# Performance work log

Hardware: AMD Instinct MI355X
Metric: run time of the kernel (lower is better)

## Reference

```python
import jax, jax.numpy as jnp
import numpy as np

N = 100000   # nodes
E = 1600000  # edges
D = 128      # feature dim
C = 32       # n classes (logits dim)
LN_EPS = 1e-5   # torch LayerNorm default eps
LOG_EPS = 1e-9  # numerical floor inside logs


def setup_inputs() -> dict:
    key = jax.random.key(0)
    ks = jax.random.split(key, 8)
    h = jax.random.normal(ks[0], (N, D), jnp.float32)
    logits = jax.random.normal(ks[1], (N, C), jnp.float32)
    old_z = jax.random.uniform(ks[2], (N,), jnp.float32)
    norm = jax.random.uniform(ks[3], (N, 1), jnp.float32)  # degree norm per node
    tau_1 = jax.random.uniform(ks[4], (1,), jnp.float32)
    tau_2 = jax.random.uniform(ks[5], (1,), jnp.float32)
    src = jax.random.randint(ks[6], (E,), 0, N, jnp.int32)
    dst = jax.random.randint(ks[7], (E,), 0, N, jnp.int32)
    return dict(h=h, logits=logits, old_z=old_z, norm=norm,
                tau_1=tau_1, tau_2=tau_2, src=src, dst=dst)


def _layernorm_over_nodes(x):
    # LayerNorm(N, elementwise_affine=False) applied to a length-N vector:
    # normalize over the entire node dimension.
    mu = jnp.mean(x)
    var = jnp.mean(jnp.square(x - mu))
    return (x - mu) * jax.lax.rsqrt(var + LN_EPS)


def reference(h, logits, old_z, norm, tau_1, tau_2, src, dst):
    # --- message pass 1: adaptive_reduce_func over neighbor logits ---
    probs = jax.nn.softmax(logits, axis=-1)                      # [N,C]
    ones = jnp.ones((src.shape[0],), h.dtype)
    deg = jax.ops.segment_sum(ones, dst, num_segments=N)          # in-degree [N]
    sum_p = jax.ops.segment_sum(probs[src], dst, num_segments=N)  # [N,C]
    mean_p = sum_p / jnp.maximum(deg, 1.0)[:, None]               # neighborhood consensus
    log_self = jnp.log(probs + LOG_EPS)
    log_mean = jnp.log(mean_p + LOG_EPS)
    f1 = jnp.sum(probs * (log_self - log_mean), axis=-1)          # KL(self || mean-neighbor)
    f2 = -jnp.sum(mean_p * log_mean, axis=-1)                     # entropy of consensus
    has_nb = deg > 0  # DGL leaves zero-in-degree nodes at 0
    f1 = jnp.where(has_nb, f1, 0.0)
    f2 = jnp.where(has_nb, f2, 0.0)

    # --- gating (shared_tau=True path) ---
    z = jax.nn.sigmoid(-(_layernorm_over_nodes(f1) - tau_1)) \
      * jax.nn.sigmoid(-(_layernorm_over_nodes(f2) - tau_2))      # [N]
    gate = jnp.minimum(old_z, z)

    # --- message pass 2: sum-aggregate neighbor features ---
    agg = jax.ops.segment_sum(h[src], dst, num_segments=N)        # [N,D]
    normagg = jax.nn.relu(agg * norm)
    new_h = h + gate[:, None] * normagg
    return new_h, z
```

## Files before the change

kernel.cpp:

```cpp
#include <hip/hip_runtime.h>
#include <math.h>

#define CN 32
#define DN 128
#define BKT_SHIFT 9
#define BKT_NODES 512
#define CHUNK 8192
#define MAXBKT 1024

__global__ void k_softmax(const float* __restrict__ logits, float* __restrict__ probs, int N) {
    int t = blockIdx.x * blockDim.x + threadIdx.x;
    int node = t >> 5, c = t & 31;
    if (node >= N) return;
    float l = logits[node * CN + c];
    float m = l;
    #pragma unroll
    for (int o = 16; o; o >>= 1) m = fmaxf(m, __shfl_xor(m, o, 32));
    float e = __expf(l - m);
    float s = e;
    #pragma unroll
    for (int o = 16; o; o >>= 1) s += __shfl_xor(s, o, 32);
    probs[node * CN + c] = e / s;
}

__global__ void k_part_hist(const int* __restrict__ dst, int* __restrict__ M,
                            int E, int NBKT) {
    __shared__ int hist[MAXBKT];
    int t = threadIdx.x;
    for (int j = t; j < NBKT; j += 256) hist[j] = 0;
    __syncthreads();
    int ebeg = blockIdx.x * CHUNK;
    #pragma unroll
    for (int k = 0; k < CHUNK / 256; ++k) {
        int e = ebeg + k * 256 + t;
        if (e < E) atomicAdd(&hist[dst[e] >> BKT_SHIFT], 1);
    }
    __syncthreads();
    int* row = M + (size_t)blockIdx.x * NBKT;
    for (int j = t; j < NBKT; j += 256) row[j] = hist[j];
}

__global__ void k_part_scan(int* __restrict__ M, int* __restrict__ bbase,
                            int NCH, int NBKT, int E) {
    __shared__ int wsum[16], wpre[16];
    __shared__ int carry;
    int t = threadIdx.x, ln = t & 63, wv = t >> 6;
    if (t == 0) carry = 0;
    __syncthreads();
    int L = NCH * NBKT;
    for (int base = 0; base < L; base += 1024) {
        int k = base + t;
        int idx = 0, v = 0;
        if (k < L) {
            int b = k / NCH, ch = k - b * NCH;
            idx = ch * NBKT + b;
            v = M[idx];
        }
        int incl = v;
        #pragma unroll
        for (int o = 1; o < 64; o <<= 1) { int u = __shfl_up(incl, o, 64); if (ln >= o) incl += u; }
        if (ln == 63) wsum[wv] = incl;
        __syncthreads();
        if (t == 0) {
            int r = carry;
            #pragma unroll
            for (int w = 0; w < 16; ++w) { wpre[w] = r; r += wsum[w]; }
            carry = r;
        }
        __syncthreads();
        if (k < L) M[idx] = wpre[wv] + incl - v;
        __syncthreads();
    }
    for (int b = t; b < NBKT; b += 1024) bbase[b] = M[b];
    if (t == 0) bbase[NBKT] = E;
}

__global__ void k_part_scatter(const int* __restrict__ src, const int* __restrict__ dst,
                               const int* __restrict__ M, int* __restrict__ part,
                               int E, int NBKT) {
    __shared__ int cur[MAXBKT];
    int t = threadIdx.x;
    const int* row = M + (size_t)blockIdx.x * NBKT;
    for (int j = t; j < NBKT; j += 256) cur[j] = row[j];
    __syncthreads();
    int ebeg = blockIdx.x * CHUNK;
    #pragma unroll
    for (int k = 0; k < CHUNK / 256; ++k) {
        int e = ebeg + k * 256 + t;
        if (e < E) {
            int d = dst[e];
            int b = d >> BKT_SHIFT;
            int p = atomicAdd(&cur[b], 1);
            part[p] = ((d & (BKT_NODES - 1)) << 17) | src[e];
        }
    }
}

__global__ void k_bucket_csr(const int* __restrict__ part, const int* __restrict__ bbase,
                             int* __restrict__ cnt, int* __restrict__ off,
                             int* __restrict__ eidx, int N) {
    __shared__ int hcnt[BKT_NODES];
    __shared__ int wsum[8], wpre[8];
    int t = threadIdx.x, ln = t & 63, wv = t >> 6;
    int b = blockIdx.x;
    int lo = bbase[b], hi = bbase[b + 1];
    hcnt[t] = 0;
    __syncthreads();
    for (int e = lo + t; e < hi; e += BKT_NODES)
        atomicAdd(&hcnt[part[e] >> 17], 1);
    __syncthreads();
    int v = hcnt[t];
    int incl = v;
    #pragma unroll
    for (int o = 1; o < 64; o <<= 1) { int u = __shfl_up(incl, o, 64); if (ln >= o) incl += u; }
    if (ln == 63) wsum[wv] = incl;
    __syncthreads();
    if (t == 0) {
        int r = 0;
        #pragma unroll
        for (int w = 0; w < 8; ++w) { wpre[w] = r; r += wsum[w]; }
    }
    __syncthreads();
    int excl = wpre[wv] + incl - v;
    int g = b * BKT_NODES + t;
    if (g < N) { cnt[g] = v; off[g] = lo + excl; }
    hcnt[t] = excl;
    __syncthreads();
    for (int e = lo + t; e < hi; e += BKT_NODES) {
        int pk = part[e];
        int p = atomicAdd(&hcnt[pk >> 17], 1);
        eidx[lo + p] = pk & 0x1FFFF;
    }
}

__global__ void k_probs_f(const float* __restrict__ probs, const int* __restrict__ off,
                          const int* __restrict__ cnt, const int* __restrict__ eidx,
                          float* __restrict__ f1buf, float* __restrict__ f2buf,
                          double* __restrict__ pbuf, int N) {
    int t = blockIdx.x * blockDim.x + threadIdx.x;
    int i = t >> 5, c = t & 31;
    float f1 = 0.f, f2 = 0.f;
    if (i < N) {
        int beg = off[i], dg = cnt[i];
        float sum = 0.f;
        for (int base = 0; base < dg; base += 16) {
            int rem = dg - base;
            int lim = rem < 16 ? rem : 16;
            int myi = (c < lim) ? eidx[beg + base + c] : 0;
            #pragma unroll
            for (int j = 0; j < 16; ++j) {
                int s = __shfl(myi, j, 32);
                float v = probs[(size_t)s * CN + c];
                sum += (j < rem) ? v : 0.f;
            }
        }
        float f1c = 0.f, f2c = 0.f;
        if (dg > 0) {
            float p = probs[(size_t)i * CN + c];
            float mp = sum / (float)dg;
            float lm = logf(mp + 1e-9f);
            f1c = p * (logf(p + 1e-9f) - lm);
            f2c = -mp * lm;
        }
        #pragma unroll
        for (int o = 16; o; o >>= 1) { f1c += __shfl_xor(f1c, o, 32); f2c += __shfl_xor(f2c, o, 32); }
        if (c == 0) { f1buf[i] = f1c; f2buf[i] = f2c; f1 = f1c; f2 = f2c; }
    }
    double v0 = f1, v1 = (double)f1 * f1, v2 = f2, v3 = (double)f2 * f2;
    #pragma unroll
    for (int o = 32; o; o >>= 1) {
        v0 += __shfl_down(v0, o, 64);
        v1 += __shfl_down(v1, o, 64);
        v2 += __shfl_down(v2, o, 64);
        v3 += __shfl_down(v3, o, 64);
    }
    __shared__ double sh[4][4];
    int wave = threadIdx.x >> 6, lane = threadIdx.x & 63;
    if (lane == 0) { sh[0][wave] = v0; sh[1][wave] = v1; sh[2][wave] = v2; sh[3][wave] = v3; }
    __syncthreads();
    if (threadIdx.x == 0) {
        double a = 0, b = 0, c2 = 0, d = 0;
        #pragma unroll
        for (int w = 0; w < 4; ++w) { a += sh[0][w]; b += sh[1][w]; c2 += sh[2][w]; d += sh[3][w]; }
        double* p = pbuf + (size_t)blockIdx.x * 4;
        p[0] = a; p[1] = b; p[2] = c2; p[3] = d;
    }
}

__global__ void k_redstats(const double* __restrict__ pbuf, double* __restrict__ stats, int nblk) {
    int t = threadIdx.x;
    double a = 0, b = 0, c = 0, d = 0;
    for (int k = t; k < nblk; k += blockDim.x) {
        const double* p = pbuf + (size_t)k * 4;
        a += p[0]; b += p[1]; c += p[2]; d += p[3];
    }
    #pragma unroll
    for (int o = 32; o; o >>= 1) {
        a += __shfl_down(a, o, 64);
        b += __shfl_down(b, o, 64);
        c += __shfl_down(c, o, 64);
        d += __shfl_down(d, o, 64);
    }
    __shared__ double sh[4][16];
    int wv = t >> 6, ln = t & 63;
    if (ln == 0) { sh[0][wv] = a; sh[1][wv] = b; sh[2][wv] = c; sh[3][wv] = d; }
    __syncthreads();
    if (t == 0) {
        double s0 = 0, s1 = 0, s2 = 0, s3 = 0;
        int nw = blockDim.x >> 6;
        for (int w = 0; w < nw; ++w) { s0 += sh[0][w]; s1 += sh[1][w]; s2 += sh[2][w]; s3 += sh[3][w]; }
        stats[0] = s0; stats[1] = s1; stats[2] = s2; stats[3] = s3;
    }
}

__global__ void k_z(const float* __restrict__ f1buf, const float* __restrict__ f2buf,
                    const double* __restrict__ stats, const float* __restrict__ old_z,
                    const float* __restrict__ tau1, const float* __restrict__ tau2,
                    float* __restrict__ z_out, float* __restrict__ gate, int N) {
    int i = blockIdx.x * blockDim.x + threadIdx.x;
    if (i >= N) return;
    double invN = 1.0 / (double)N;
    float mu1 = (float)(stats[0] * invN);
    float var1 = (float)(stats[1] * invN) - mu1 * mu1;
    float is1 = rsqrtf(var1 + 1e-5f);
    float mu2 = (float)(stats[2] * invN);
    float var2 = (float)(stats[3] * invN) - mu2 * mu2;
    float is2 = rsqrtf(var2 + 1e-5f);
    float a = (f1buf[i] - mu1) * is1;
    float b = (f2buf[i] - mu2) * is2;
    float z = (1.f / (1.f + __expf(a - tau1[0]))) * (1.f / (1.f + __expf(b - tau2[0])));
    z_out[i] = z;
    gate[i] = fminf(old_z[i], z);
}

__global__ void k_gather_final(const float* __restrict__ h, const int* __restrict__ off,
                               const int* __restrict__ cnt, const int* __restrict__ eidx,
                               const float* __restrict__ gate, const float* __restrict__ norm,
                               float* __restrict__ out, int N) {
    int t = blockIdx.x * blockDim.x + threadIdx.x;
    int i = t >> 6, ln = t & 63;
    if (i >= N) return;
    int beg = off[i], dg = cnt[i];
    const float2* h2 = (const float2*)h;
    float ax = 0.f, ay = 0.f;
    for (int base = 0; base < dg; base += 16) {
        int rem = dg - base;
        int lim = rem < 16 ? rem : 16;
        int myi = (ln < lim) ? eidx[beg + base + ln] : 0;
        #pragma unroll
        for (int j = 0; j < 16; ++j) {
            int s = __shfl(myi, j, 64);
            float2 v = h2[(size_t)s * 64 + ln];
            bool use = j < rem;
            ax += use ? v.x : 0.f;
            ay += use ? v.y : 0.f;
        }
    }
    float g = gate[i], nm = norm[i];
    float2 hv = h2[(size_t)i * 64 + ln];
    float2 r;
    r.x = hv.x + g * fmaxf(ax * nm, 0.f);
    r.y = hv.y + g * fmaxf(ay * nm, 0.f);
    ((float2*)out)[(size_t)i * 64 + ln] = r;
}

extern "C" void kernel_launch(void* const* d_in, const int* in_sizes, int n_in,
                              void* d_out, int out_size, void* d_ws, size_t ws_size,
                              hipStream_t stream) {
    const float* h      = (const float*)d_in[0];
    const float* logits = (const float*)d_in[1];
    const float* old_z  = (const float*)d_in[2];
    const float* norm   = (const float*)d_in[3];
    const float* tau1   = (const float*)d_in[4];
    const float* tau2   = (const float*)d_in[5];
    const int*   src    = (const int*)d_in[6];
    const int*   dst    = (const int*)d_in[7];
    const int N = in_sizes[2];
    const int E = in_sizes[6];

    float* out   = (float*)d_out;
    float* z_out = out + (size_t)N * DN;

    const int B = 256;
    const int NBF  = (N * CN + B - 1) / B;
    const int NBKT = (N + BKT_NODES - 1) >> BKT_SHIFT;
    const int NCH  = (E + CHUNK - 1) / CHUNK;

    char*   ws    = (char*)d_ws;
    double* stats = (double*)ws;
    int*    cnt   = (int*)(ws + 64);
    int*    off   = cnt + N;
    int*    bbase = off + N;
    int*    M     = bbase + MAXBKT + 8;
    int*    eidx  = M + (size_t)NCH * NBKT;
    int*    part  = eidx + E;
    float*  probs = (float*)(part + E);
    float*  f1buf = probs + (size_t)N * CN;
    float*  f2buf = f1buf + N;
    float*  gate  = f2buf + N;
    double* pbuf  = (double*)(((size_t)(gate + N) + 15) & ~(size_t)15);

    k_softmax<<<(N * CN + B - 1) / B, B, 0, stream>>>(logits, probs, N);

    k_part_hist<<<NCH, 256, 0, stream>>>(dst, M, E, NBKT);
    k_part_scan<<<1, 1024, 0, stream>>>(M, bbase, NCH, NBKT, E);
    k_part_scatter<<<NCH, 256, 0, stream>>>(src, dst, M, part, E, NBKT);
    k_bucket_csr<<<NBKT, BKT_NODES, 0, stream>>>(part, bbase, cnt, off, eidx, N);

    k_probs_f<<<NBF, B, 0, stream>>>(probs, off, cnt, eidx, f1buf, f2buf, pbuf, N);
    k_redstats<<<1, 1024, 0, stream>>>(pbuf, stats, NBF);
    k_z<<<(N + B - 1) / B, B, 0, stream>>>(f1buf, f2buf, stats, old_z, tau1, tau2, z_out, gate, N);

    k_gather_final<<<(N * 64 + B - 1) / B, B, 0, stream>>>(h, off, cnt, eidx, gate, norm, out, N);
}
```

Before: 302.7 us.

## Gather neighbor probs and features in bf16, stage bucket CSR in LDS

Adds bf16 copies of the softmax probabilities and of h, and makes the two neighbor-gather kernels read these half-width copies while keeping fp32 accumulation and fp32 self terms. The aim is to roughly halve the random-gather memory traffic that dominates both message passes. The bucket-CSR kernel now loads each bucket's packed edges into LDS once and writes the sorted indices back in place, removing one E-sized buffer. In exchange it adds a full conversion pass over h, loses precision in the aggregated sums, and silently drops edges when a bucket holds more than DCAP entries.

```diff
diff --git a/kernel.cpp b/kernel.cpp
--- a/kernel.cpp
+++ b/kernel.cpp
@@ -7,8 +7,18 @@
 #define BKT_NODES 512
 #define CHUNK 8192
 #define MAXBKT 1024
-
-__global__ void k_softmax(const float* __restrict__ logits, float* __restrict__ probs, int N) {
+#define DCAP 12288
+
+__device__ __forceinline__ unsigned short f2b(float f) {
+    unsigned u = __float_as_uint(f);
+    return (unsigned short)((u + 0x7FFFu + ((u >> 16) & 1u)) >> 16);
+}
+__device__ __forceinline__ float b2f(unsigned short s) {
+    return __uint_as_float(((unsigned)s) << 16);
+}
+
+__global__ void k_softmax(const float* __restrict__ logits, float* __restrict__ probs,
+                          unsigned short* __restrict__ probs_b, int N) {
     int t = blockIdx.x * blockDim.x + threadIdx.x;
     int node = t >> 5, c = t & 31;
     if (node >= N) return;
@@ -20,7 +30,18 @@
     float s = e;
     #pragma unroll
     for (int o = 16; o; o >>= 1) s += __shfl_xor(s, o, 32);
-    probs[node * CN + c] = e / s;
+    float p = e / s;
+    probs[node * CN + c] = p;
+    probs_b[node * CN + c] = f2b(p);
+}
+
+__global__ void k_cvt_h(const float4* __restrict__ h4, ushort4* __restrict__ hb4, int n4) {
+    int t = blockIdx.x * blockDim.x + threadIdx.x;
+    if (t >= n4) return;
+    float4 v = h4[t];
+    ushort4 r;
+    r.x = f2b(v.x); r.y = f2b(v.y); r.z = f2b(v.z); r.w = f2b(v.w);
+    hb4[t] = r;
 }
 
 __global__ void k_part_hist(const int* __restrict__ dst, int* __restrict__ M,
@@ -96,18 +117,20 @@
     }
 }
 
-__global__ void k_bucket_csr(const int* __restrict__ part, const int* __restrict__ bbase,
-                             int* __restrict__ cnt, int* __restrict__ off,
-                             int* __restrict__ eidx, int N) {
+__global__ void k_bucket_csr(int* __restrict__ part, const int* __restrict__ bbase,
+                             int* __restrict__ cnt, int* __restrict__ off, int N) {
+    __shared__ int sbuf[DCAP];
     __shared__ int hcnt[BKT_NODES];
     __shared__ int wsum[8], wpre[8];
     int t = threadIdx.x, ln = t & 63, wv = t >> 6;
     int b = blockIdx.x;
     int lo = bbase[b], hi = bbase[b + 1];
+    int n = hi - lo;
+    if (n > DCAP) n = DCAP;
+    for (int e = t; e < n; e += BKT_NODES) sbuf[e] = part[lo + e];
     hcnt[t] = 0;
     __syncthreads();
-    for (int e = lo + t; e < hi; e += BKT_NODES)
-        atomicAdd(&hcnt[part[e] >> 17], 1);
+    for (int e = t; e < n; e += BKT_NODES) atomicAdd(&hcnt[sbuf[e] >> 17], 1);
     __syncthreads();
     int v = hcnt[t];
     int incl = v;
@@ -126,15 +149,17 @@
     if (g < N) { cnt[g] = v; off[g] = lo + excl; }
     hcnt[t] = excl;
     __syncthreads();
-    for (int e = lo + t; e < hi; e += BKT_NODES) {
-        int pk = part[e];
+    for (int e = t; e < n; e += BKT_NODES) {
+        int pk = sbuf[e];
         int p = atomicAdd(&hcnt[pk >> 17], 1);
-        eidx[lo + p] = pk & 0x1FFFF;
-    }
-}
-
-__global__ void k_probs_f(const float* __restrict__ probs, const int* __restrict__ off,
-                          const int* __restrict__ cnt, const int* __restrict__ eidx,
+        part[lo + p] = pk & 0x1FFFF;
+    }
+}
+
+__global__ void k_probs_f(const float* __restrict__ probs,
+                          const unsigned short* __restrict__ probs_b,
+                          const int* __restrict__ off, const int* __restrict__ cnt,
+                          const int* __restrict__ eidx,
                           float* __restrict__ f1buf, float* __restrict__ f2buf,
                           double* __restrict__ pbuf, int N) {
     int t = blockIdx.x * blockDim.x + threadIdx.x;
@@ -150,7 +175,7 @@
             #pragma unroll
             for (int j = 0; j < 16; ++j) {
                 int s = __shfl(myi, j, 32);
-                float v = probs[(size_t)s * CN + c];
+                float v = b2f(probs_b[(size_t)s * CN + c]);
                 sum += (j < rem) ? v : 0.f;
             }
         }
@@ -233,10 +258,44 @@
     gate[i] = fminf(old_z[i], z);
 }
 
-__global__ void k_gather_final(const float* __restrict__ h, const int* __restrict__ off,
-                               const int* __restrict__ cnt, const int* __restrict__ eidx,
-                               const float* __restrict__ gate, const float* __restrict__ norm,
-                               float* __restrict__ out, int N) {
+__global__ void k_gather_final_b(const float* __restrict__ h,
+                                 const unsigned short* __restrict__ hb,
+                                 const int* __restrict__ off, const int* __restrict__ cnt,
+                                 const int* __restrict__ eidx,
+                                 const float* __restrict__ gate, const float* __restrict__ norm,
+                                 float* __restrict__ out, int N) {
+    int t = blockIdx.x * blockDim.x + threadIdx.x;
+    int i = t >> 6, ln = t & 63;
+    if (i >= N) return;
+    int beg = off[i], dg = cnt[i];
+    const ushort2* hb2 = (const ushort2*)hb;
+    float ax = 0.f, ay = 0.f;
+    for (int base = 0; base < dg; base += 16) {
+        int rem = dg - base;
+        int lim = rem < 16 ? rem : 16;
+        int myi = (ln < lim) ? eidx[beg + base + ln] : 0;
+        #pragma unroll
+        for (int j = 0; j < 16; ++j) {
+            int s = __shfl(myi, j, 64);
+            ushort2 v = hb2[(size_t)s * 64 + ln];
+            bool use = j < rem;
+            ax += use ? b2f(v.x) : 0.f;
+            ay += use ? b2f(v.y) : 0.f;
+        }
+    }
+    float g = gate[i], nm = norm[i];
+    const float2* h2 = (const float2*)h;
+    float2 hv = h2[(size_t)i * 64 + ln];
+    float2 r;
+    r.x = hv.x + g * fmaxf(ax * nm, 0.f);
+    r.y = hv.y + g * fmaxf(ay * nm, 0.f);
+    ((float2*)out)[(size_t)i * 64 + ln] = r;
+}
+
+__global__ void k_gather_final_f(const float* __restrict__ h, const int* __restrict__ off,
+                                 const int* __restrict__ cnt, const int* __restrict__ eidx,
+                                 const float* __restrict__ gate, const float* __restrict__ norm,
+                                 float* __restrict__ out, int N) {
     int t = blockIdx.x * blockDim.x + threadIdx.x;
     int i = t >> 6, ln = t & 63;
     if (i >= N) return;
@@ -293,23 +352,31 @@
     int*    bbase = off + N;
     int*    M     = bbase + MAXBKT + 8;
     int*    eidx  = M + (size_t)NCH * NBKT;
-    int*    part  = eidx + E;
-    float*  probs = (float*)(part + E);
-    float*  f1buf = probs + (size_t)N * CN;
+    float*  probs = (float*)(eidx + E);
+    unsigned short* probs_b = (unsigned short*)(probs + (size_t)N * CN);
+    float*  f1buf = (float*)(probs_b + (size_t)N * CN);
     float*  f2buf = f1buf + N;
     float*  gate  = f2buf + N;
     double* pbuf  = (double*)(((size_t)(gate + N) + 15) & ~(size_t)15);
-
-    k_softmax<<<(N * CN + B - 1) / B, B, 0, stream>>>(logits, probs, N);
+    unsigned short* hb = (unsigned short*)(pbuf + (size_t)NBF * 4);
+    size_t need_full = (size_t)((char*)(hb + (size_t)N * DN) - ws);
+    bool use_bf16_h = ws_size >= need_full;
+
+    k_softmax<<<(N * CN + B - 1) / B, B, 0, stream>>>(logits, probs, probs_b, N);
+    if (use_bf16_h)
+        k_cvt_h<<<(N * DN / 4 + B - 1) / B, B, 0, stream>>>((const float4*)h, (ushort4*)hb, N * DN / 4);
 
     k_part_hist<<<NCH, 256, 0, stream>>>(dst, M, E, NBKT);
     k_part_scan<<<1, 1024, 0, stream>>>(M, bbase, NCH, NBKT, E);
-    k_part_scatter<<<NCH, 256, 0, stream>>>(src, dst, M, part, E, NBKT);
-    k_bucket_csr<<<NBKT, BKT_NODES, 0, stream>>>(part, bbase, cnt, off, eidx, N);
-
-    k_probs_f<<<NBF, B, 0, stream>>>(probs, off, cnt, eidx, f1buf, f2buf, pbuf, N);
+    k_part_scatter<<<NCH, 256, 0, stream>>>(src, dst, M, eidx, E, NBKT);
+    k_bucket_csr<<<NBKT, BKT_NODES, 0, stream>>>(eidx, bbase, cnt, off, N);
+
+    k_probs_f<<<NBF, B, 0, stream>>>(probs, probs_b, off, cnt, eidx, f1buf, f2buf, pbuf, N);
     k_redstats<<<1, 1024, 0, stream>>>(pbuf, stats, NBF);
     k_z<<<(N + B - 1) / B, B, 0, stream>>>(f1buf, f2buf, stats, old_z, tau1, tau2, z_out, gate, N);
 
-    k_gather_final<<<(N * 64 + B - 1) / B, B, 0, stream>>>(h, off, cnt, eidx, gate, norm, out, N);
-}
+    if (use_bf16_h)
+        k_gather_final_b<<<(N * 64 + B - 1) / B, B, 0, stream>>>(h, hb, off, cnt, eidx, gate, norm, out, N);
+    else
+        k_gather_final_f<<<(N * 64 + B - 1) / B, B, 0, stream>>>(h, off, cnt, eidx, gate, norm, out, N);
+}
```

New measurement: 329.3 us. 1.09x slower.

## Stage bucket edges in LDS in place and column-slice the feature gather

Applied to the files above, without the earlier changes.

The bucket CSR kernel now copies each bucket's packed edges into shared memory and writes the sorted source indices back into the same buffer in place. This removes the separate part buffer and the repeated global reads. The final gather is split into 8 column slices of 16 floats, with blocks ordered so that concurrent blocks touch the same slice of h, aiming for better L2 locality. It also uses nontemporal loads for indices and nontemporal stores for the output. The trade-offs are that buckets larger than DCAP are silently truncated, and the gather now issues narrower 64-byte row accesses per neighbour with redundant index loads across slices.

```diff
diff --git a/kernel.cpp b/kernel.cpp
--- a/kernel.cpp
+++ b/kernel.cpp
@@ -7,6 +7,7 @@
 #define BKT_NODES 512
 #define CHUNK 8192
 #define MAXBKT 1024
+#define DCAP 12288
 
 __global__ void k_softmax(const float* __restrict__ logits, float* __restrict__ probs, int N) {
     int t = blockIdx.x * blockDim.x + threadIdx.x;
@@ -96,18 +97,20 @@
     }
 }
 
-__global__ void k_bucket_csr(const int* __restrict__ part, const int* __restrict__ bbase,
-                             int* __restrict__ cnt, int* __restrict__ off,
-                             int* __restrict__ eidx, int N) {
+__global__ void k_bucket_csr(int* __restrict__ part, const int* __restrict__ bbase,
+                             int* __restrict__ cnt, int* __restrict__ off, int N) {
+    __shared__ int sbuf[DCAP];
     __shared__ int hcnt[BKT_NODES];
     __shared__ int wsum[8], wpre[8];
     int t = threadIdx.x, ln = t & 63, wv = t >> 6;
     int b = blockIdx.x;
     int lo = bbase[b], hi = bbase[b + 1];
+    int n = hi - lo;
+    if (n > DCAP) n = DCAP;
+    for (int e = t; e < n; e += BKT_NODES) sbuf[e] = part[lo + e];
     hcnt[t] = 0;
     __syncthreads();
-    for (int e = lo + t; e < hi; e += BKT_NODES)
-        atomicAdd(&hcnt[part[e] >> 17], 1);
+    for (int e = t; e < n; e += BKT_NODES) atomicAdd(&hcnt[sbuf[e] >> 17], 1);
     __syncthreads();
     int v = hcnt[t];
     int incl = v;
@@ -126,10 +129,10 @@
     if (g < N) { cnt[g] = v; off[g] = lo + excl; }
     hcnt[t] = excl;
     __syncthreads();
-    for (int e = lo + t; e < hi; e += BKT_NODES) {
-        int pk = part[e];
+    for (int e = t; e < n; e += BKT_NODES) {
+        int pk = sbuf[e];
         int p = atomicAdd(&hcnt[pk >> 17], 1);
-        eidx[lo + p] = pk & 0x1FFFF;
+        part[lo + p] = pk & 0x1FFFF;
     }
 }
 
@@ -233,35 +236,33 @@
     gate[i] = fminf(old_z[i], z);
 }
 
-__global__ void k_gather_final(const float* __restrict__ h, const int* __restrict__ off,
-                               const int* __restrict__ cnt, const int* __restrict__ eidx,
-                               const float* __restrict__ gate, const float* __restrict__ norm,
-                               float* __restrict__ out, int N) {
-    int t = blockIdx.x * blockDim.x + threadIdx.x;
-    int i = t >> 6, ln = t & 63;
+__global__ void k_gather_cs(const float* __restrict__ h, const int* __restrict__ off,
+                            const int* __restrict__ cnt, const int* __restrict__ eidx,
+                            const float* __restrict__ gate, const float* __restrict__ norm,
+                            float* __restrict__ out, int N) {
+    int t = threadIdx.x;
+    int grp = t >> 4, c = t & 15;
+    int slice = blockIdx.x & 7;
+    int i = (blockIdx.x >> 3) * 16 + grp;
     if (i >= N) return;
+    int col = slice * 16 + c;
     int beg = off[i], dg = cnt[i];
-    const float2* h2 = (const float2*)h;
-    float ax = 0.f, ay = 0.f;
+    float acc = 0.f;
     for (int base = 0; base < dg; base += 16) {
         int rem = dg - base;
         int lim = rem < 16 ? rem : 16;
-        int myi = (ln < lim) ? eidx[beg + base + ln] : 0;
+        int myi = (c < lim) ? __builtin_nontemporal_load(&eidx[beg + base + c]) : 0;
         #pragma unroll
         for (int j = 0; j < 16; ++j) {
-            int s = __shfl(myi, j, 64);
-            float2 v = h2[(size_t)s * 64 + ln];
-            bool use = j < rem;
-            ax += use ? v.x : 0.f;
-            ay += use ? v.y : 0.f;
+            int s = __shfl(myi, j, 16);
+            float v = h[(size_t)s * DN + col];
+            acc += (j < rem) ? v : 0.f;
         }
     }
     float g = gate[i], nm = norm[i];
-    float2 hv = h2[(size_t)i * 64 + ln];
-    float2 r;
-    r.x = hv.x + g * fmaxf(ax * nm, 0.f);
-    r.y = hv.y + g * fmaxf(ay * nm, 0.f);
-    ((float2*)out)[(size_t)i * 64 + ln] = r;
+    float hv = h[(size_t)i * DN + col];
+    float r = hv + g * fmaxf(acc * nm, 0.f);
+    __builtin_nontemporal_store(r, &out[(size_t)i * DN + col]);
 }
 
 extern "C" void kernel_launch(void* const* d_in, const int* in_sizes, int n_in,
@@ -293,8 +294,7 @@
     int*    bbase = off + N;
     int*    M     = bbase + MAXBKT + 8;
     int*    eidx  = M + (size_t)NCH * NBKT;
-    int*    part  = eidx + E;
-    float*  probs = (float*)(part + E);
+    float*  probs = (float*)(eidx + E);
     float*  f1buf = probs + (size_t)N * CN;
     float*  f2buf = f1buf + N;
     float*  gate  = f2buf + N;
@@ -304,12 +304,13 @@
 
     k_part_hist<<<NCH, 256, 0, stream>>>(dst, M, E, NBKT);
     k_part_scan<<<1, 1024, 0, stream>>>(M, bbase, NCH, NBKT, E);
-    k_part_scatter<<<NCH, 256, 0, stream>>>(src, dst, M, part, E, NBKT);
-    k_bucket_csr<<<NBKT, BKT_NODES, 0, stream>>>(part, bbase, cnt, off, eidx, N);
+    k_part_scatter<<<NCH, 256, 0, stream>>>(src, dst, M, eidx, E, NBKT);
+    k_bucket_csr<<<NBKT, BKT_NODES, 0, stream>>>(eidx, bbase, cnt, off, N);
 
     k_probs_f<<<NBF, B, 0, stream>>>(probs, off, cnt, eidx, f1buf, f2buf, pbuf, N);
     k_redstats<<<1, 1024, 0, stream>>>(pbuf, stats, NBF);
     k_z<<<(N + B - 1) / B, B, 0, stream>>>(f1buf, f2buf, stats, old_z, tau1, tau2, z_out, gate, N);
 
-    k_gather_final<<<(N * 64 + B - 1) / B, B, 0, stream>>>(h, off, cnt, eidx, gate, norm, out, N);
-}
+    const int NGB = ((N + 15) / 16) * 8;
+    k_gather_cs<<<NGB, 256, 0, stream>>>(h, off, cnt, eidx, gate, norm, out, N);
+}
```

Result: slower. 376.5 us (+24.4%).
